# Performance work log

Measured on AMD Instinct MI355X. Metric: run time of the kernel, lower is better.

The kernel has to match this reference:

```python
import jax, jax.numpy as jnp
import numpy as np

NUM_HEADS = 16
HEAD_DIM = 64  # embedding_dim 1024 / 16


def setup_inputs() -> dict:
    key = jax.random.key(0)
    k1, k2, k3, k4 = jax.random.split(key, 4)
    B, S, D = 2, 2048, 1024
    return {
        "query": jax.random.normal(k1, (B, S, D), dtype=jnp.float32),
        "key": jax.random.normal(k2, (B, S, D), dtype=jnp.float32),
        "value": jax.random.normal(k3, (B, S, D), dtype=jnp.float32),
        "W_out": jax.random.normal(k4, (D, D), dtype=jnp.float32) * (1.0 / np.sqrt(D)),
        "b_out": jnp.zeros((D,), dtype=jnp.float32),
    }


def reference(query, key, value, W_out, b_out):
    B, S, D = query.shape
    H, hd = NUM_HEADS, HEAD_DIM
    # NOTE: original forward never applies q_fc/k_fc/v_fc (transform ignores fc)
    q = query.reshape(B, S, H, hd).transpose(0, 2, 1, 3)  # [B,H,S,hd]
    k = key.reshape(B, S, H, hd).transpose(0, 2, 1, 3)
    v = value.reshape(B, S, H, hd).transpose(0, 2, 1, 3)
    scores = jnp.einsum("bhqd,bhkd->bhqk", q, k) / jnp.sqrt(jnp.float32(hd))
    probs = jax.nn.softmax(scores, axis=-1)  # mask=None, dropout=None
    ctx = jnp.einsum("bhqk,bhkd->bhqd", probs, v)
    ctx = ctx.transpose(0, 2, 1, 3).reshape(B, S, D)
    return ctx @ W_out.T + b_out
```

## Files before the change

kernel.cpp:

```cpp
#include <hip/hip_runtime.h>
#include <hip/hip_bf16.h>
#include <stdint.h>

#define NB 2
#define SEQ 2048
#define DIM 1024
#define NH 16
#define HD 64

typedef __attribute__((ext_vector_type(4))) float f32x4;
typedef __attribute__((ext_vector_type(16))) float f32x16;
typedef __attribute__((ext_vector_type(8))) short s16x8;
typedef __attribute__((ext_vector_type(4))) short s16x4;
typedef __attribute__((ext_vector_type(8))) __bf16 bf16x8;

static __device__ __forceinline__ short f2bf_rne(float x) {
  uint32_t u = __float_as_uint(x);
  u += 0x7fffu + ((u >> 16) & 1u);
  return (short)(u >> 16);
}
static __device__ __forceinline__ uint32_t pk_bf16(float a, float b) {
  __hip_bfloat162 h = __float22bfloat162_rn(float2{a, b});
  uint32_t u;
  __builtin_memcpy(&u, &h, 4);
  return u;
}
static __device__ __forceinline__ bf16x8 ldfrag(const short* p) {
  bf16x8 r;
  __builtin_memcpy(&r, p, 16);
  return r;
}
static __device__ __forceinline__ void glds16(const short* g, short* l) {
  __builtin_amdgcn_global_load_lds(
      (const __attribute__((address_space(1))) uint32_t*)g,
      (__attribute__((address_space(3))) uint32_t*)l, 16, 0, 0);
}

__global__ __launch_bounds__(256) void prep_all(const float* __restrict__ K,
                                                const float* __restrict__ V,
                                                const float* __restrict__ W,
                                                short* __restrict__ Kh,
                                                short* __restrict__ Vt,
                                                short* __restrict__ Wh) {
  __shared__ float vtile[64][65];
  const int tid = threadIdx.x;
  const int id = blockIdx.x;

  if (id >= 1024) {
    size_t idx = ((size_t)(id - 1024) * 256 + tid) * 8;
    f32x4 a = *(const f32x4*)(W + idx);
    f32x4 b = *(const f32x4*)(W + idx + 4);
    s16x8 o;
#pragma unroll
    for (int j = 0; j < 4; ++j) {
      o[j] = f2bf_rne(a[j]);
      o[4 + j] = f2bf_rne(b[j]);
    }
    *(s16x8*)(Wh + idx) = o;
    return;
  }

  const int t0 = (id & 31) * 64;
  const int bh = id >> 5;
  const int b = bh >> 4, h = bh & 15;

#pragma unroll
  for (int i = 0; i < 4; ++i) {
    int f = tid + 256 * i;
    int row = f >> 4;
    int col = (f & 15) * 4;
    const float* src = K + ((size_t)(b * SEQ + t0 + row)) * DIM + h * HD + col;
    f32x4 v = *(const f32x4*)src;
    s16x4 hi;
#pragma unroll
    for (int j = 0; j < 4; ++j) hi[j] = f2bf_rne(v[j]);
    *(s16x4*)(Kh + ((size_t)bh * SEQ + t0 + row) * HD + col) = hi;
  }
#pragma unroll
  for (int i = 0; i < 4; ++i) {
    int f = tid + 256 * i;
    int row = f >> 4;
    int col = (f & 15) * 4;
    const float* src = V + ((size_t)(b * SEQ + t0 + row)) * DIM + h * HD + col;
    f32x4 v = *(const f32x4*)src;
#pragma unroll
    for (int j = 0; j < 4; ++j) vtile[row][col + j] = v[j];
  }
  __syncthreads();
#pragma unroll
  for (int i = 0; i < 4; ++i) {
    int idx = tid + 256 * i;
    int d = idx >> 4;
    int kb = (idx & 15) * 4;
    int kp = (kb & ~12) | ((kb & 4) << 1) | ((kb & 8) >> 1);
    s16x4 o4;
#pragma unroll
    for (int j = 0; j < 4; ++j) o4[j] = f2bf_rne(vtile[kb + j][d]);
    *(s16x4*)(Vt + ((size_t)bh * HD + d) * SEQ + t0 + kp) = o4;
  }
}

#define QSCALE (0.125f * 1.44269504088896340736f)

__global__ __launch_bounds__(512, 4) void attn(const float* __restrict__ Q,
                                               const short* __restrict__ Kh,
                                               const short* __restrict__ Vt,
                                               short* __restrict__ Ch) {
  __shared__ __align__(16) short smem[32768];

  const int tid = threadIdx.x;
  const int wv = tid >> 6, ln = tid & 63;
  const int grp = wv >> 2, wl = wv & 3;
  const int l32 = ln & 31, hl = ln >> 5;
  const int bh = blockIdx.y, b = bh >> 4, hh = bh & 15;
  const int q0 = blockIdx.x * 128 + wl * 32;

  short* kt0 = smem + grp * 2 * 4096;
  short* kt1 = smem + (grp * 2 + 1) * 4096;
  short* vt0 = smem + 16384 + grp * 2 * 4096;
  short* vt1 = smem + 16384 + (grp * 2 + 1) * 4096;

  bf16x8 qh[4];
  {
    const float* qp = Q + ((size_t)(b * SEQ + q0 + l32)) * DIM + hh * HD + hl * 8;
#pragma unroll
    for (int ks = 0; ks < 4; ++ks) {
      short th[8];
#pragma unroll
      for (int j = 0; j < 8; ++j) th[j] = f2bf_rne(qp[ks * 16 + j] * QSCALE);
      __builtin_memcpy(&qh[ks], th, 16);
    }
  }

  f32x16 acc[2];
#pragma unroll
  for (int r = 0; r < 16; ++r) {
    acc[0][r] = 0.f;
    acc[1][r] = 0.f;
  }
  float den0 = 0.f, den1 = 0.f;

  const short* khg = Kh + (size_t)bh * SEQ * HD;
  const short* vtg = Vt + (size_t)bh * HD * SEQ;

  const int srow8 = ln >> 3;
  const int sg = ln & 7;
  const int sw = (sg ^ srow8) * 8;

  {
    const int kv0 = grp * 64;
#pragma unroll
    for (int i = 0; i < 4; ++i) {
      int c = wl * 4 + i;
      int row = (c & 7) * 8 + srow8;
      if (c < 8)
        glds16(khg + (size_t)(kv0 + row) * HD + sw, kt0 + (c & 7) * 512);
      else
        glds16(vtg + (size_t)row * SEQ + kv0 + sw, vt0 + (c & 7) * 512);
    }
  }

  for (int t = 0; t < 16; ++t) {
    __syncthreads();
    if (t + 1 < 16) {
      const int kvn = (2 * (t + 1) + grp) * 64;
      short* kd = ((t + 1) & 1) ? kt1 : kt0;
      short* vd = ((t + 1) & 1) ? vt1 : vt0;
#pragma unroll
      for (int i = 0; i < 4; ++i) {
        int c = wl * 4 + i;
        int row = (c & 7) * 8 + srow8;
        if (c < 8)
          glds16(khg + (size_t)(kvn + row) * HD + sw, kd + (c & 7) * 512);
        else
          glds16(vtg + (size_t)row * SEQ + kvn + sw, vd + (c & 7) * 512);
      }
    }
    const short* kb = (t & 1) ? kt1 : kt0;
    const short* vbuf = (t & 1) ? vt1 : vt0;

#pragma unroll
    for (int nt = 0; nt < 2; ++nt) {
      f32x16 sf;
#pragma unroll
      for (int r = 0; r < 16; ++r) sf[r] = 0.f;
#pragma unroll
      for (int ks = 0; ks < 4; ++ks) {
        bf16x8 kf =
            ldfrag(kb + (nt * 32 + l32) * 64 + (((ks * 2 + hl) ^ (l32 & 7)) * 8));
        sf = __builtin_amdgcn_mfma_f32_32x32x16_bf16(kf, qh[ks], sf, 0, 0, 0);
      }
#pragma unroll
      for (int tp = 0; tp < 2; ++tp) {
        uint32_t w[4];
#pragma unroll
        for (int j2 = 0; j2 < 4; ++j2) {
          float p0 = __builtin_amdgcn_exp2f(sf[tp * 8 + j2 * 2]);
          float p1 = __builtin_amdgcn_exp2f(sf[tp * 8 + j2 * 2 + 1]);
          den0 += p0;
          den1 += p1;
          w[j2] = pk_bf16(p0, p1);
        }
        bf16x8 pa;
        __builtin_memcpy(&pa, w, 16);
        const int ksg = nt * 2 + tp;
#pragma unroll
        for (int dt = 0; dt < 2; ++dt) {
          bf16x8 vf = ldfrag(vbuf + (dt * 32 + l32) * 64 +
                             (((ksg * 2 + hl) ^ (l32 & 7)) * 8));
          acc[dt] =
              __builtin_amdgcn_mfma_f32_32x32x16_bf16(pa, vf, acc[dt], 0, 0, 0);
        }
      }
    }
  }

  __syncthreads();
  f32x4* R4 = (f32x4*)smem;
  float* Rd = (float*)smem + 8192;
  if (grp == 1) {
#pragma unroll
    for (int dt = 0; dt < 2; ++dt)
#pragma unroll
      for (int j = 0; j < 4; ++j) {
        f32x4 v = {acc[dt][j * 4 + 0], acc[dt][j * 4 + 1], acc[dt][j * 4 + 2],
                   acc[dt][j * 4 + 3]};
        R4[(wl * 8 + dt * 4 + j) * 64 + ln] = v;
      }
    Rd[wl * 64 + ln] = den0 + den1;
  }
  __syncthreads();
  if (grp == 0) {
    float den = den0 + den1 + Rd[wl * 64 + ln];
#pragma unroll
    for (int dt = 0; dt < 2; ++dt)
#pragma unroll
      for (int j = 0; j < 4; ++j) {
        f32x4 v = R4[(wl * 8 + dt * 4 + j) * 64 + ln];
#pragma unroll
        for (int e = 0; e < 4; ++e) acc[dt][j * 4 + e] += v[e];
      }
    den += __shfl_xor(den, 32);
    float invd = 1.0f / den;
    float inv_r[16];
#pragma unroll
    for (int r = 0; r < 16; ++r)
      inv_r[r] = __shfl(invd, (r & 3) + 8 * (r >> 2) + 4 * hl, 64);
#pragma unroll
    for (int dt = 0; dt < 2; ++dt)
#pragma unroll
      for (int r = 0; r < 16; ++r) {
        int row = (r & 3) + 8 * (r >> 2) + 4 * hl;
        size_t off =
            ((size_t)(b * SEQ + q0 + row)) * DIM + hh * HD + dt * 32 + l32;
        Ch[off] = f2bf_rne(acc[dt][r] * inv_r[r]);
      }
  }
}

__global__ __launch_bounds__(256, 4) void proj(const short* __restrict__ Ah,
                                               const short* __restrict__ Wh,
                                               const float* __restrict__ bias,
                                               float* __restrict__ OUT) {
  __shared__ __align__(16) short ash[2][4096];
  __shared__ __align__(16) short wsh[2][4096];
  const int tid = threadIdx.x;
  const int wv = tid >> 6, ln = tid & 63;
  const int l32 = ln & 31, hl = ln >> 5;
  const int wm = wv & 1, wn = wv >> 1;
  const int m0 = blockIdx.x * 64, n0 = blockIdx.y * 64;

  f32x16 acc;
#pragma unroll
  for (int r = 0; r < 16; ++r) acc[r] = 0.f;

  const int srow8 = ln >> 3, sg = ln & 7;
  const int sw = (sg ^ srow8) * 8;

#pragma unroll
  for (int i = 0; i < 4; ++i) {
    int c = wv * 4 + i;
    int row = (c & 7) * 8 + srow8;
    if (c < 8)
      glds16(Ah + (size_t)(m0 + row) * DIM + sw, ash[0] + (c & 7) * 512);
    else
      glds16(Wh + (size_t)(n0 + row) * DIM + sw, wsh[0] + (c & 7) * 512);
  }

  for (int kt = 0; kt < DIM / 64; ++kt) {
    __syncthreads();
    if (kt + 1 < DIM / 64) {
      const int kk = (kt + 1) * 64;
      const int bn = (kt + 1) & 1;
#pragma unroll
      for (int i = 0; i < 4; ++i) {
        int c = wv * 4 + i;
        int row = (c & 7) * 8 + srow8;
        if (c < 8)
          glds16(Ah + (size_t)(m0 + row) * DIM + kk + sw, ash[bn] + (c & 7) * 512);
        else
          glds16(Wh + (size_t)(n0 + row) * DIM + kk + sw, wsh[bn] + (c & 7) * 512);
      }
    }
    const short* ab = ash[kt & 1];
    const short* wb = wsh[kt & 1];
#pragma unroll
    for (int ks = 0; ks < 4; ++ks) {
      bf16x8 af = ldfrag(ab + (wm * 32 + l32) * 64 + (((ks * 2 + hl) ^ (l32 & 7)) * 8));
      bf16x8 wf = ldfrag(wb + (wn * 32 + l32) * 64 + (((ks * 2 + hl) ^ (l32 & 7)) * 8));
      acc = __builtin_amdgcn_mfma_f32_32x32x16_bf16(af, wf, acc, 0, 0, 0);
    }
  }

  float bs = bias[n0 + wn * 32 + l32];
#pragma unroll
  for (int r = 0; r < 16; ++r) {
    int row = m0 + wm * 32 + (r & 3) + 8 * (r >> 2) + 4 * hl;
    int col = n0 + wn * 32 + l32;
    OUT[(size_t)row * DIM + col] = acc[r] + bs;
  }
}

extern "C" void kernel_launch(void* const* d_in, const int* in_sizes, int n_in,
                              void* d_out, int out_size, void* d_ws, size_t ws_size,
                              hipStream_t stream) {
  const float* Q = (const float*)d_in[0];
  const float* K = (const float*)d_in[1];
  const float* V = (const float*)d_in[2];
  const float* W = (const float*)d_in[3];
  const float* bias = (const float*)d_in[4];
  float* OUT = (float*)d_out;

  char* ws = (char*)d_ws;
  short* Kh = (short*)(ws + ((size_t)0 << 20));
  short* Vt = (short*)(ws + ((size_t)8 << 20));
  short* Ch = (short*)(ws + ((size_t)16 << 20));
  short* Wh = (short*)(ws + ((size_t)24 << 20));

  prep_all<<<dim3(1536), 256, 0, stream>>>(K, V, W, Kh, Vt, Wh);
  attn<<<dim3(SEQ / 128, NB * NH), 512, 0, stream>>>(Q, Kh, Vt, Ch);
  proj<<<dim3((NB * SEQ) / 64, DIM / 64), 256, 0, stream>>>(Ch, Wh, bias, OUT);
}
```

Baseline: 162.7 us.

## Software-pipeline QK^T one tile ahead and drop the split-KV wave groups

The attention kernel goes from 512 threads with two wave groups that each handle half the KV sequence (then reduce through LDS) to 256 threads that each walk the full KV range. The QK^T scores for the next tile are computed while the current tile's exp and PV MFMAs run, with K prefetched two tiles ahead and V one tile ahead. This removes the cross-group LDS reduction and its extra syncs, and lets score MFMAs overlap the softmax VALU work. In exchange it uses more registers for the extra score accumulators, and the smaller blocks with launch bounds of 2 may lower occupancy.

```diff
diff --git a/kernel.cpp b/kernel.cpp
--- a/kernel.cpp
+++ b/kernel.cpp
@@ -101,24 +101,20 @@
 }
 
 #define QSCALE (0.125f * 1.44269504088896340736f)
-
-__global__ __launch_bounds__(512, 4) void attn(const float* __restrict__ Q,
+#define NT_KV 32
+
+__global__ __launch_bounds__(256, 2) void attn(const float* __restrict__ Q,
                                                const short* __restrict__ Kh,
                                                const short* __restrict__ Vt,
                                                short* __restrict__ Ch) {
-  __shared__ __align__(16) short smem[32768];
+  __shared__ __align__(16) short kbuf[2][4096];
+  __shared__ __align__(16) short vbuf[2][4096];
 
   const int tid = threadIdx.x;
   const int wv = tid >> 6, ln = tid & 63;
-  const int grp = wv >> 2, wl = wv & 3;
   const int l32 = ln & 31, hl = ln >> 5;
   const int bh = blockIdx.y, b = bh >> 4, hh = bh & 15;
-  const int q0 = blockIdx.x * 128 + wl * 32;
-
-  short* kt0 = smem + grp * 2 * 4096;
-  short* kt1 = smem + (grp * 2 + 1) * 4096;
-  short* vt0 = smem + 16384 + grp * 2 * 4096;
-  short* vt1 = smem + 16384 + (grp * 2 + 1) * 4096;
+  const int q0 = blockIdx.x * 128 + wv * 32;
 
   bf16x8 qh[4];
   {
@@ -147,56 +143,76 @@
   const int sg = ln & 7;
   const int sw = (sg ^ srow8) * 8;
 
-  {
-    const int kv0 = grp * 64;
-#pragma unroll
-    for (int i = 0; i < 4; ++i) {
-      int c = wl * 4 + i;
-      int row = (c & 7) * 8 + srow8;
-      if (c < 8)
-        glds16(khg + (size_t)(kv0 + row) * HD + sw, kt0 + (c & 7) * 512);
-      else
-        glds16(vtg + (size_t)row * SEQ + kv0 + sw, vt0 + (c & 7) * 512);
-    }
-  }
-
-  for (int t = 0; t < 16; ++t) {
+#pragma unroll
+  for (int i = 0; i < 6; ++i) {
+    int c = wv * 6 + i;
+    int lc = c & 7;
+    int row = lc * 8 + srow8;
+    if (c < 8)
+      glds16(khg + (size_t)row * HD + sw, &kbuf[0][lc * 512]);
+    else if (c < 16)
+      glds16(vtg + (size_t)row * SEQ + sw, &vbuf[0][lc * 512]);
+    else
+      glds16(khg + (size_t)(64 + row) * HD + sw, &kbuf[1][lc * 512]);
+  }
+  __syncthreads();
+
+  f32x16 sf[2];
+#pragma unroll
+  for (int nt = 0; nt < 2; ++nt) {
+#pragma unroll
+    for (int r = 0; r < 16; ++r) sf[nt][r] = 0.f;
+#pragma unroll
+    for (int ks = 0; ks < 4; ++ks) {
+      bf16x8 kf = ldfrag(&kbuf[0][0] + (nt * 32 + l32) * 64 +
+                         (((ks * 2 + hl) ^ (l32 & 7)) * 8));
+      sf[nt] = __builtin_amdgcn_mfma_f32_32x32x16_bf16(kf, qh[ks], sf[nt], 0, 0, 0);
+    }
+  }
+
+  for (int t = 0; t < NT_KV; ++t) {
     __syncthreads();
-    if (t + 1 < 16) {
-      const int kvn = (2 * (t + 1) + grp) * 64;
-      short* kd = ((t + 1) & 1) ? kt1 : kt0;
-      short* vd = ((t + 1) & 1) ? vt1 : vt0;
-#pragma unroll
-      for (int i = 0; i < 4; ++i) {
-        int c = wl * 4 + i;
-        int row = (c & 7) * 8 + srow8;
-        if (c < 8)
-          glds16(khg + (size_t)(kvn + row) * HD + sw, kd + (c & 7) * 512);
-        else
-          glds16(vtg + (size_t)row * SEQ + kvn + sw, vd + (c & 7) * 512);
-      }
-    }
-    const short* kb = (t & 1) ? kt1 : kt0;
-    const short* vbuf = (t & 1) ? vt1 : vt0;
+    if (t + 2 < NT_KV) {
+      const int kvn = (t + 2) * 64;
+#pragma unroll
+      for (int i = 0; i < 2; ++i) {
+        int lc = wv * 2 + i;
+        int row = lc * 8 + srow8;
+        glds16(khg + (size_t)(kvn + row) * HD + sw, &kbuf[t & 1][lc * 512]);
+      }
+    }
+    if (t + 1 < NT_KV) {
+      const int kvn = (t + 1) * 64;
+#pragma unroll
+      for (int i = 0; i < 2; ++i) {
+        int lc = wv * 2 + i;
+        int row = lc * 8 + srow8;
+        glds16(vtg + (size_t)row * SEQ + kvn + sw, &vbuf[(t + 1) & 1][lc * 512]);
+      }
+    }
+    const short* kbn = &kbuf[(t + 1) & 1][0];
+    const short* vbc = &vbuf[t & 1][0];
 
 #pragma unroll
     for (int nt = 0; nt < 2; ++nt) {
-      f32x16 sf;
-#pragma unroll
-      for (int r = 0; r < 16; ++r) sf[r] = 0.f;
-#pragma unroll
-      for (int ks = 0; ks < 4; ++ks) {
-        bf16x8 kf =
-            ldfrag(kb + (nt * 32 + l32) * 64 + (((ks * 2 + hl) ^ (l32 & 7)) * 8));
-        sf = __builtin_amdgcn_mfma_f32_32x32x16_bf16(kf, qh[ks], sf, 0, 0, 0);
+      f32x16 sfn;
+      if (t + 1 < NT_KV) {
+#pragma unroll
+        for (int r = 0; r < 16; ++r) sfn[r] = 0.f;
+#pragma unroll
+        for (int ks = 0; ks < 4; ++ks) {
+          bf16x8 kf = ldfrag(kbn + (nt * 32 + l32) * 64 +
+                             (((ks * 2 + hl) ^ (l32 & 7)) * 8));
+          sfn = __builtin_amdgcn_mfma_f32_32x32x16_bf16(kf, qh[ks], sfn, 0, 0, 0);
+        }
       }
 #pragma unroll
       for (int tp = 0; tp < 2; ++tp) {
         uint32_t w[4];
 #pragma unroll
         for (int j2 = 0; j2 < 4; ++j2) {
-          float p0 = __builtin_amdgcn_exp2f(sf[tp * 8 + j2 * 2]);
-          float p1 = __builtin_amdgcn_exp2f(sf[tp * 8 + j2 * 2 + 1]);
+          float p0 = __builtin_amdgcn_exp2f(sf[nt][tp * 8 + j2 * 2]);
+          float p1 = __builtin_amdgcn_exp2f(sf[nt][tp * 8 + j2 * 2 + 1]);
           den0 += p0;
           den1 += p1;
           w[j2] = pk_bf16(p0, p1);
@@ -206,56 +222,31 @@
         const int ksg = nt * 2 + tp;
 #pragma unroll
         for (int dt = 0; dt < 2; ++dt) {
-          bf16x8 vf = ldfrag(vbuf + (dt * 32 + l32) * 64 +
+          bf16x8 vf = ldfrag(vbc + (dt * 32 + l32) * 64 +
                              (((ksg * 2 + hl) ^ (l32 & 7)) * 8));
           acc[dt] =
               __builtin_amdgcn_mfma_f32_32x32x16_bf16(pa, vf, acc[dt], 0, 0, 0);
         }
       }
-    }
-  }
-
-  __syncthreads();
-  f32x4* R4 = (f32x4*)smem;
-  float* Rd = (float*)smem + 8192;
-  if (grp == 1) {
-#pragma unroll
-    for (int dt = 0; dt < 2; ++dt)
-#pragma unroll
-      for (int j = 0; j < 4; ++j) {
-        f32x4 v = {acc[dt][j * 4 + 0], acc[dt][j * 4 + 1], acc[dt][j * 4 + 2],
-                   acc[dt][j * 4 + 3]};
-        R4[(wl * 8 + dt * 4 + j) * 64 + ln] = v;
-      }
-    Rd[wl * 64 + ln] = den0 + den1;
-  }
-  __syncthreads();
-  if (grp == 0) {
-    float den = den0 + den1 + Rd[wl * 64 + ln];
-#pragma unroll
-    for (int dt = 0; dt < 2; ++dt)
-#pragma unroll
-      for (int j = 0; j < 4; ++j) {
-        f32x4 v = R4[(wl * 8 + dt * 4 + j) * 64 + ln];
-#pragma unroll
-        for (int e = 0; e < 4; ++e) acc[dt][j * 4 + e] += v[e];
-      }
-    den += __shfl_xor(den, 32);
-    float invd = 1.0f / den;
-    float inv_r[16];
-#pragma unroll
-    for (int r = 0; r < 16; ++r)
-      inv_r[r] = __shfl(invd, (r & 3) + 8 * (r >> 2) + 4 * hl, 64);
-#pragma unroll
-    for (int dt = 0; dt < 2; ++dt)
-#pragma unroll
-      for (int r = 0; r < 16; ++r) {
-        int row = (r & 3) + 8 * (r >> 2) + 4 * hl;
-        size_t off =
-            ((size_t)(b * SEQ + q0 + row)) * DIM + hh * HD + dt * 32 + l32;
-        Ch[off] = f2bf_rne(acc[dt][r] * inv_r[r]);
-      }
-  }
+      if (t + 1 < NT_KV) sf[nt] = sfn;
+    }
+  }
+
+  float den = den0 + den1;
+  den += __shfl_xor(den, 32);
+  float invd = 1.0f / den;
+  float inv_r[16];
+#pragma unroll
+  for (int r = 0; r < 16; ++r)
+    inv_r[r] = __shfl(invd, (r & 3) + 8 * (r >> 2) + 4 * hl, 64);
+#pragma unroll
+  for (int dt = 0; dt < 2; ++dt)
+#pragma unroll
+    for (int r = 0; r < 16; ++r) {
+      int row = (r & 3) + 8 * (r >> 2) + 4 * hl;
+      size_t off = ((size_t)(b * SEQ + q0 + row)) * DIM + hh * HD + dt * 32 + l32;
+      Ch[off] = f2bf_rne(acc[dt][r] * inv_r[r]);
+    }
 }
 
 __global__ __launch_bounds__(256, 4) void proj(const short* __restrict__ Ah,
@@ -338,6 +329,6 @@
   short* Wh = (short*)(ws + ((size_t)24 << 20));
 
   prep_all<<<dim3(1536), 256, 0, stream>>>(K, V, W, Kh, Vt, Wh);
-  attn<<<dim3(SEQ / 128, NB * NH), 512, 0, stream>>>(Q, Kh, Vt, Ch);
+  attn<<<dim3(SEQ / 128, NB * NH), 256, 0, stream>>>(Q, Kh, Vt, Ch);
   proj<<<dim3((NB * SEQ) / 64, DIM / 64), 256, 0, stream>>>(Ch, Wh, bias, OUT);
 }
```

Result: faster. 159.1 us (-2.2%).
